# Kernel tuning notes

Measured on AMD Instinct MI355X. Metric: run time of the kernel, lower is better.

## Reference

```python
import jax, jax.numpy as jnp
import numpy as np

N_HEADS = 16
D_MODEL = 1024
D_K = 64
D_V = 64


def setup_inputs() -> dict:
    key = jax.random.key(0)
    ks = jax.random.split(key, 12)
    B, S = 2, 2048
    s = 0.02
    return {
        "q": jax.random.normal(ks[0], (B, S, D_MODEL), jnp.float32),
        "k": jax.random.normal(ks[1], (B, S, D_MODEL), jnp.float32),
        "v": jax.random.normal(ks[2], (B, S, D_MODEL), jnp.float32),
        "bias": jax.random.normal(ks[3], (B, N_HEADS, S, S), jnp.float32),
        "w_q": jax.random.normal(ks[4], (D_MODEL, N_HEADS * D_K), jnp.float32) * s,
        "b_q": jnp.zeros((N_HEADS * D_K,), jnp.float32),
        "w_k": jax.random.normal(ks[5], (D_MODEL, N_HEADS * D_K), jnp.float32) * s,
        "b_k": jnp.zeros((N_HEADS * D_K,), jnp.float32),
        "w_v": jax.random.normal(ks[6], (D_MODEL, N_HEADS * D_V), jnp.float32) * s,
        "b_v": jnp.zeros((N_HEADS * D_V,), jnp.float32),
        "w_o": jax.random.normal(ks[7], (D_MODEL, D_MODEL), jnp.float32) * s,
        "b_o": jnp.zeros((D_MODEL,), jnp.float32),
    }


def reference(q, k, v, bias, w_q, b_q, w_k, b_k, w_v, b_v, w_o, b_o):
    B, Sq, _ = q.shape
    Sk = k.shape[1]
    # QKV projections -> [B, H, S, d]
    qh = (q @ w_q + b_q).reshape(B, Sq, N_HEADS, D_K).transpose(0, 2, 1, 3)
    kh = (k @ w_k + b_k).reshape(B, Sk, N_HEADS, D_K).transpose(0, 2, 1, 3)
    vh = (v @ w_v + b_v).reshape(B, Sk, N_HEADS, D_V).transpose(0, 2, 1, 3)
    scale = 1.0 / jnp.sqrt(jnp.asarray(D_K, qh.dtype))
    attn = jnp.einsum("bhqd,bhkd->bhqk", qh * scale, kh) + bias
    weights = jax.nn.softmax(attn, axis=-1)  # dropout=0 -> identity
    out = jnp.einsum("bhqk,bhkd->bhqd", weights, vh)
    out = out.transpose(0, 2, 1, 3).reshape(B, Sq, N_HEADS * D_V)
    return out @ w_o + b_o
```

## Files before the change

### kernel.cpp

```cpp
#include <hip/hip_runtime.h>
#include <stdint.h>

#define H_ 16
#define B_ 2
#define S_ 2048
#define DMODEL 1024
#define MTOT 4096

typedef __attribute__((ext_vector_type(8))) __bf16 bf16x8;
typedef __attribute__((ext_vector_type(4))) float f32x4;
typedef unsigned short ushort_t;

typedef __attribute__((address_space(1))) uint32_t u32_g;
typedef __attribute__((address_space(3))) uint32_t u32_l;

static __device__ __forceinline__ unsigned short f2bf(float f) {
  union { float f; uint32_t u; } x; x.f = f;
  uint32_t r = (x.u + 0x7FFFu + ((x.u >> 16) & 1u)) >> 16;
  return (unsigned short)r;
}

static __device__ __forceinline__ void gld_lds16(const void* g, void* l) {
  __builtin_amdgcn_global_load_lds((const u32_g*)g, (u32_l*)l, 16, 0, 0);
}

__global__ __launch_bounds__(256) void cast_qkv(const float* __restrict__ q,
                                                const float* __restrict__ k,
                                                const float* __restrict__ v,
                                                ushort_t* qb, ushort_t* kb, ushort_t* vb) {
  int z = blockIdx.y;
  const float* src = (z == 0) ? q : (z == 1) ? k : v;
  ushort_t* dst = (z == 0) ? qb : (z == 1) ? kb : vb;
  int idx = (blockIdx.x * 256 + threadIdx.x) * 4;
  float4 f = *(const float4*)(src + idx);
  ushort4 o;
  o.x = f2bf(f.x); o.y = f2bf(f.y); o.z = f2bf(f.z); o.w = f2bf(f.w);
  *(ushort4*)(dst + idx) = o;
}

__global__ __launch_bounds__(256) void transw(const float* __restrict__ wq, const float* __restrict__ wk,
                                              const float* __restrict__ wv, const float* __restrict__ wo,
                                              ushort_t* tq, ushort_t* tk, ushort_t* tv, ushort_t* tow) {
  int z = blockIdx.y;
  const float* src = (z == 0) ? wq : (z == 1) ? wk : (z == 2) ? wv : wo;
  ushort_t* dst = (z == 0) ? tq : (z == 1) ? tk : (z == 2) ? tv : tow;
  __shared__ ushort_t lds[64 * 65];
  int t = threadIdx.x;
  int k0 = (blockIdx.x & 15) * 64;
  int n0 = (blockIdx.x >> 4) * 64;
  int r = t >> 4;
  int c4 = (t & 15) * 4;
#pragma unroll
  for (int j = 0; j < 4; ++j) {
    int row = j * 16 + r;
    float4 f = *(const float4*)(src + (size_t)(k0 + row) * DMODEL + n0 + c4);
    lds[(c4 + 0) * 65 + row] = f2bf(f.x);
    lds[(c4 + 1) * 65 + row] = f2bf(f.y);
    lds[(c4 + 2) * 65 + row] = f2bf(f.z);
    lds[(c4 + 3) * 65 + row] = f2bf(f.w);
  }
  __syncthreads();
  int nn = t >> 2;
  int kb = (t & 3) * 16;
  ushort_t tmp[16];
#pragma unroll
  for (int j = 0; j < 16; ++j) tmp[j] = lds[nn * 65 + kb + j];
  ushort_t* dp = dst + (size_t)(n0 + nn) * DMODEL + k0 + kb;
  *(uint4*)(dp + 0) = *(const uint4*)(tmp + 0);
  *(uint4*)(dp + 8) = *(const uint4*)(tmp + 8);
}

struct GemmArgs {
  const ushort_t* A;
  const ushort_t* Bt;
  const float* bias;
  void* out;
  int mode;
  float mult;
};

__global__ __launch_bounds__(256) void gemm128(GemmArgs g0, GemmArgs g1, GemmArgs g2) {
  GemmArgs ga = (blockIdx.z == 0) ? g0 : (blockIdx.z == 1) ? g1 : g2;
  __shared__ alignas(16) ushort_t smem[2][128 * 64];
  ushort_t* As = smem[0];
  ushort_t* Bs = smem[1];
  int tid = threadIdx.x, wid = tid >> 6, lane = tid & 63;
  int lg = lane >> 4, li = lane & 15;
  int wr = wid >> 1, wc = wid & 1;
  int m0 = blockIdx.y * 128, n0 = blockIdx.x * 128;
  f32x4 acc[4][4] = {};
  const ushort_t* Ab = ga.A + (size_t)m0 * DMODEL;
  const ushort_t* Bb = ga.Bt + (size_t)n0 * DMODEL;

  for (int kt = 0; kt < DMODEL / 64; ++kt) {
    int k0 = kt * 64;
    __syncthreads();
#pragma unroll
    for (int r = 0; r < 4; ++r) {
      int c = r * 256 + tid;
      int row = c >> 3, off = (c & 7) * 8;
      gld_lds16(Ab + row * DMODEL + k0 + off, (char*)As + c * 16);
      gld_lds16(Bb + row * DMODEL + k0 + off, (char*)Bs + c * 16);
    }
    __syncthreads();
#pragma unroll
    for (int kk = 0; kk < 2; ++kk) {
      bf16x8 af[4], bfr[4];
#pragma unroll
      for (int x = 0; x < 4; ++x) {
        af[x]  = *(const bf16x8*)(As + (wr * 64 + x * 16 + li) * 64 + kk * 32 + lg * 8);
        bfr[x] = *(const bf16x8*)(Bs + (wc * 64 + x * 16 + li) * 64 + kk * 32 + lg * 8);
      }
#pragma unroll
      for (int mi = 0; mi < 4; ++mi)
#pragma unroll
        for (int ni = 0; ni < 4; ++ni)
          acc[mi][ni] = __builtin_amdgcn_mfma_f32_16x16x32_bf16(af[mi], bfr[ni], acc[mi][ni], 0, 0, 0);
    }
  }

  if (ga.mode == 1) {
    __syncthreads();
    ushort_t* ep = &smem[0][0];
#pragma unroll
    for (int mi = 0; mi < 4; ++mi)
#pragma unroll
      for (int ni = 0; ni < 4; ++ni) {
        int nl = wc * 64 + ni * 16 + li;
        float bv = ga.bias[n0 + nl];
#pragma unroll
        for (int i = 0; i < 4; ++i) {
          int ml = wr * 64 + mi * 16 + lg * 4 + i;
          ep[nl * 128 + ml] = f2bf((acc[mi][ni][i] + bv) * ga.mult);
        }
      }
    __syncthreads();
    int row = tid >> 1;
    int cg  = (tid & 1) * 64;
    int n = n0 + row;
    int h = n >> 6, d = n & 63;
    int b = m0 >> 11;
    size_t base = ((size_t)(b * H_ + h) * 64 + d) * S_ + (m0 & 2047) + cg;
    ushort_t* out = (ushort_t*)ga.out;
    const ushort_t* sp = ep + row * 128 + cg;
#pragma unroll
    for (int j = 0; j < 8; ++j)
      *(uint4*)(out + base + j * 8) = *(const uint4*)(sp + j * 8);
  } else {
#pragma unroll
    for (int mi = 0; mi < 4; ++mi) {
#pragma unroll
      for (int ni = 0; ni < 4; ++ni) {
        int n = n0 + wc * 64 + ni * 16 + li;
        float bv = ga.bias[n];
#pragma unroll
        for (int i = 0; i < 4; ++i) {
          int m = m0 + wr * 64 + mi * 16 + lg * 4 + i;
          float val = (acc[mi][ni][i] + bv) * ga.mult;
          if (ga.mode == 2) {
            ((float*)ga.out)[(size_t)m * DMODEL + n] = val;
          } else {
            int b = m >> 11, s = m & 2047;
            int h = n >> 6, d = n & 63;
            size_t addr = ((size_t)(b * H_ + h) * S_ + s) * 64 + d;
            ((ushort_t*)ga.out)[addr] = f2bf(val);
          }
        }
      }
    }
  }
}

__global__ __launch_bounds__(256, 4) void attn(const ushort_t* __restrict__ Qh,
                                               const ushort_t* __restrict__ Kh,
                                               const ushort_t* __restrict__ VhT,
                                               const float* __restrict__ bias,
                                               ushort_t* __restrict__ attnO) {
  int qt = blockIdx.x * 64;
  int h = blockIdx.y, b = blockIdx.z;
  int tid = threadIdx.x, wid = tid >> 6, lane = tid & 63;
  int lg = lane >> 4, li = lane & 15;
  __shared__ alignas(16) ushort_t Ks[2][64 * 64];
  __shared__ alignas(16) ushort_t Vts[2][64 * 64];
  __shared__ alignas(16) ushort_t Ps[4][16][64];

  const size_t bh = (size_t)(b * H_ + h);
  const ushort_t* Qbase = Qh + bh * S_ * 64;
  const ushort_t* Kbase = Kh + bh * S_ * 64;
  const ushort_t* Vbase = VhT + bh * 64 * S_;
  const float* biasb = bias + bh * (size_t)S_ * S_;
  const int qrow = qt + wid * 16 + lg * 4;

  bf16x8 qf[2];
#pragma unroll
  for (int kk = 0; kk < 2; ++kk)
    qf[kk] = *(const bf16x8*)(Qbase + (size_t)(qt + wid * 16 + li) * 64 + kk * 32 + lg * 8);

  auto stage = [&](int buf, int t) {
#pragma unroll
    for (int r = 0; r < 2; ++r) {
      int cc = r * 256 + tid;
      int row = cc >> 3, off = (cc & 7) * 8;
      gld_lds16(Kbase + (size_t)(t * 64 + row) * 64 + off, (char*)Ks[buf] + cc * 16);
      gld_lds16(Vbase + (size_t)row * S_ + t * 64 + off, (char*)Vts[buf] + cc * 16);
    }
  };
  auto biasld = [&](float (&dst)[4][4], int t) {
#pragma unroll
    for (int n = 0; n < 4; ++n)
#pragma unroll
      for (int i = 0; i < 4; ++i)
        dst[n][i] = biasb[(size_t)(qrow + i) * S_ + t * 64 + n * 16 + li];
  };

  f32x4 o[4] = {};
  float mrow[4] = {-3.0e38f, -3.0e38f, -3.0e38f, -3.0e38f};
  float lrow[4] = {0.f, 0.f, 0.f, 0.f};
  float bsvN[4][4], bsvC[4][4];

  stage(0, 0);
  biasld(bsvN, 0);

  for (int t = 0; t < S_ / 64; ++t) {
    __syncthreads();
#pragma unroll
    for (int n = 0; n < 4; ++n)
#pragma unroll
      for (int i = 0; i < 4; ++i)
        bsvC[n][i] = bsvN[n][i];
    if (t + 1 < S_ / 64) {
      stage((t + 1) & 1, t + 1);
      biasld(bsvN, t + 1);
    }
    const ushort_t* Kc = Ks[t & 1];
    const ushort_t* Vc = Vts[t & 1];

    f32x4 sc[4] = {};
#pragma unroll
    for (int kk = 0; kk < 2; ++kk) {
#pragma unroll
      for (int n = 0; n < 4; ++n) {
        bf16x8 bk = *(const bf16x8*)(Kc + (n * 16 + li) * 64 + kk * 32 + lg * 8);
        sc[n] = __builtin_amdgcn_mfma_f32_16x16x32_bf16(qf[kk], bk, sc[n], 0, 0, 0);
      }
    }
#pragma unroll
    for (int n = 0; n < 4; ++n)
#pragma unroll
      for (int i = 0; i < 4; ++i)
        sc[n][i] += bsvC[n][i];

    float p[4][4];
#pragma unroll
    for (int i = 0; i < 4; ++i) {
      float tm = fmaxf(fmaxf(sc[0][i], sc[1][i]), fmaxf(sc[2][i], sc[3][i]));
#pragma unroll
      for (int w = 1; w < 16; w <<= 1) tm = fmaxf(tm, __shfl_xor(tm, w));
      float mn = fmaxf(mrow[i], tm);
      float alpha = __expf(mrow[i] - mn);
      float rs = 0.f;
#pragma unroll
      for (int n = 0; n < 4; ++n) { p[n][i] = __expf(sc[n][i] - mn); rs += p[n][i]; }
#pragma unroll
      for (int w = 1; w < 16; w <<= 1) rs += __shfl_xor(rs, w);
      lrow[i] = lrow[i] * alpha + rs;
      mrow[i] = mn;
#pragma unroll
      for (int n = 0; n < 4; ++n) o[n][i] *= alpha;
    }

#pragma unroll
    for (int n = 0; n < 4; ++n)
#pragma unroll
      for (int i = 0; i < 4; ++i)
        Ps[wid][lg * 4 + i][n * 16 + li] = f2bf(p[n][i]);

#pragma unroll
    for (int kk = 0; kk < 2; ++kk) {
      bf16x8 pa = *(const bf16x8*)(&Ps[wid][li][kk * 32 + lg * 8]);
#pragma unroll
      for (int n = 0; n < 4; ++n) {
        bf16x8 bv = *(const bf16x8*)(Vc + (n * 16 + li) * 64 + kk * 32 + lg * 8);
        o[n] = __builtin_amdgcn_mfma_f32_16x16x32_bf16(pa, bv, o[n], 0, 0, 0);
      }
    }
  }

  float rinv[4];
#pragma unroll
  for (int i = 0; i < 4; ++i) rinv[i] = 1.0f / lrow[i];
#pragma unroll
  for (int n = 0; n < 4; ++n)
#pragma unroll
    for (int i = 0; i < 4; ++i) {
      int q = qt + wid * 16 + lg * 4 + i;
      int col = h * 64 + n * 16 + li;
      attnO[(size_t)(b * S_ + q) * DMODEL + col] = f2bf(o[n][i] * rinv[i]);
    }
}

extern "C" void kernel_launch(void* const* d_in, const int* in_sizes, int n_in,
                              void* d_out, int out_size, void* d_ws, size_t ws_size,
                              hipStream_t stream) {
  const float* q    = (const float*)d_in[0];
  const float* k    = (const float*)d_in[1];
  const float* v    = (const float*)d_in[2];
  const float* bias = (const float*)d_in[3];
  const float* w_q  = (const float*)d_in[4];
  const float* b_q  = (const float*)d_in[5];
  const float* w_k  = (const float*)d_in[6];
  const float* b_k  = (const float*)d_in[7];
  const float* w_v  = (const float*)d_in[8];
  const float* b_v  = (const float*)d_in[9];
  const float* w_o  = (const float*)d_in[10];
  const float* b_o  = (const float*)d_in[11];

  char* ws = (char*)d_ws;
  const size_t MB = 1ull << 20;
  ushort_t* qb  = (ushort_t*)(ws + 0 * MB);
  ushort_t* kb  = (ushort_t*)(ws + 8 * MB);
  ushort_t* vb  = (ushort_t*)(ws + 16 * MB);
  ushort_t* wqT = (ushort_t*)(ws + 24 * MB);
  ushort_t* wkT = (ushort_t*)(ws + 26 * MB);
  ushort_t* wvT = (ushort_t*)(ws + 28 * MB);
  ushort_t* woT = (ushort_t*)(ws + 30 * MB);
  ushort_t* Qh  = (ushort_t*)(ws + 32 * MB);
  ushort_t* Kh  = (ushort_t*)(ws + 40 * MB);
  ushort_t* VhT = (ushort_t*)(ws + 48 * MB);
  ushort_t* aO  = qb;

  cast_qkv<<<dim3(4096, 3, 1), 256, 0, stream>>>(q, k, v, qb, kb, vb);
  transw<<<dim3(256, 4, 1), 256, 0, stream>>>(w_q, w_k, w_v, w_o, wqT, wkT, wvT, woT);

  GemmArgs gq { qb, wqT, b_q, (void*)Qh,  0, 0.125f };
  GemmArgs gk { kb, wkT, b_k, (void*)Kh,  0, 1.0f };
  GemmArgs gv { vb, wvT, b_v, (void*)VhT, 1, 1.0f };
  gemm128<<<dim3(8, 32, 3), 256, 0, stream>>>(gq, gk, gv);

  attn<<<dim3(32, 16, 2), 256, 0, stream>>>(Qh, Kh, VhT, bias, aO);

  GemmArgs go { aO, woT, b_o, d_out, 2, 1.0f };
  gemm128<<<dim3(8, 32, 1), 256, 0, stream>>>(go, go, go);
}
```

Before: 884.3 us.

## XOR-swizzle attention LDS tiles and add dedicated output-projection GEMM kernel

The attention kernel now XOR-swizzles the K, V and P shared-memory tiles by row, applied both on the global-to-LDS loads and on the MFMA fragment reads. This is meant to remove LDS bank conflicts on the 16-byte fragment reads. The output projection moves from the generic 128x128 GEMM to a new 64x128-tile kernel, which doubles the block count (512 blocks) for better occupancy. The new kernel has no double buffering, and the generic GEMM loses its fp32 output mode.

Result: no change. 881.9 us (-0.3%).

```diff
diff --git a/kernel.cpp b/kernel.cpp
--- a/kernel.cpp
+++ b/kernel.cpp
@@ -157,18 +157,73 @@
         for (int i = 0; i < 4; ++i) {
           int m = m0 + wr * 64 + mi * 16 + lg * 4 + i;
           float val = (acc[mi][ni][i] + bv) * ga.mult;
-          if (ga.mode == 2) {
-            ((float*)ga.out)[(size_t)m * DMODEL + n] = val;
-          } else {
-            int b = m >> 11, s = m & 2047;
-            int h = n >> 6, d = n & 63;
-            size_t addr = ((size_t)(b * H_ + h) * S_ + s) * 64 + d;
-            ((ushort_t*)ga.out)[addr] = f2bf(val);
-          }
+          int b = m >> 11, s = m & 2047;
+          int h = n >> 6, d = n & 63;
+          size_t addr = ((size_t)(b * H_ + h) * S_ + s) * 64 + d;
+          ((ushort_t*)ga.out)[addr] = f2bf(val);
         }
       }
     }
   }
+}
+
+__global__ __launch_bounds__(256) void gemm_out(const ushort_t* __restrict__ A,
+                                                const ushort_t* __restrict__ Bt,
+                                                const float* __restrict__ bias,
+                                                float* __restrict__ out) {
+  __shared__ alignas(16) ushort_t As[64 * 64];
+  __shared__ alignas(16) ushort_t Bs[128 * 64];
+  int tid = threadIdx.x, wid = tid >> 6, lane = tid & 63;
+  int lg = lane >> 4, li = lane & 15;
+  int m0 = blockIdx.y * 64, n0 = blockIdx.x * 128;
+  f32x4 acc[4][2] = {};
+  const ushort_t* Ab = A + (size_t)m0 * DMODEL;
+  const ushort_t* Bb = Bt + (size_t)n0 * DMODEL;
+
+  for (int kt = 0; kt < DMODEL / 64; ++kt) {
+    int k0 = kt * 64;
+    __syncthreads();
+#pragma unroll
+    for (int r = 0; r < 2; ++r) {
+      int c = r * 256 + tid;
+      int row = c >> 3, off = (c & 7) * 8;
+      gld_lds16(Ab + row * DMODEL + k0 + off, (char*)As + c * 16);
+    }
+#pragma unroll
+    for (int r = 0; r < 4; ++r) {
+      int c = r * 256 + tid;
+      int row = c >> 3, off = (c & 7) * 8;
+      gld_lds16(Bb + row * DMODEL + k0 + off, (char*)Bs + c * 16);
+    }
+    __syncthreads();
+#pragma unroll
+    for (int kk = 0; kk < 2; ++kk) {
+      bf16x8 af[4], bfr[2];
+#pragma unroll
+      for (int x = 0; x < 4; ++x)
+        af[x] = *(const bf16x8*)(As + (x * 16 + li) * 64 + kk * 32 + lg * 8);
+#pragma unroll
+      for (int x = 0; x < 2; ++x)
+        bfr[x] = *(const bf16x8*)(Bs + (wid * 32 + x * 16 + li) * 64 + kk * 32 + lg * 8);
+#pragma unroll
+      for (int mi = 0; mi < 4; ++mi)
+#pragma unroll
+        for (int ni = 0; ni < 2; ++ni)
+          acc[mi][ni] = __builtin_amdgcn_mfma_f32_16x16x32_bf16(af[mi], bfr[ni], acc[mi][ni], 0, 0, 0);
+    }
+  }
+#pragma unroll
+  for (int mi = 0; mi < 4; ++mi)
+#pragma unroll
+    for (int ni = 0; ni < 2; ++ni) {
+      int n = n0 + wid * 32 + ni * 16 + li;
+      float bv = bias[n];
+#pragma unroll
+      for (int i = 0; i < 4; ++i) {
+        int m = m0 + mi * 16 + lg * 4 + i;
+        out[(size_t)m * DMODEL + n] = acc[mi][ni][i] + bv;
+      }
+    }
 }
 
 __global__ __launch_bounds__(256, 4) void attn(const ushort_t* __restrict__ Qh,
@@ -182,7 +237,7 @@
   int lg = lane >> 4, li = lane & 15;
   __shared__ alignas(16) ushort_t Ks[2][64 * 64];
   __shared__ alignas(16) ushort_t Vts[2][64 * 64];
-  __shared__ alignas(16) ushort_t Ps[4][16][64];
+  __shared__ alignas(16) ushort_t Ps[4 * 16 * 64];
 
   const size_t bh = (size_t)(b * H_ + h);
   const ushort_t* Qbase = Qh + bh * S_ * 64;
@@ -200,7 +255,8 @@
 #pragma unroll
     for (int r = 0; r < 2; ++r) {
       int cc = r * 256 + tid;
-      int row = cc >> 3, off = (cc & 7) * 8;
+      int row = cc >> 3;
+      int off = ((cc & 7) ^ (row & 7)) * 8;
       gld_lds16(Kbase + (size_t)(t * 64 + row) * 64 + off, (char*)Ks[buf] + cc * 16);
       gld_lds16(Vbase + (size_t)row * S_ + t * 64 + off, (char*)Vts[buf] + cc * 16);
     }
@@ -240,7 +296,8 @@
     for (int kk = 0; kk < 2; ++kk) {
 #pragma unroll
       for (int n = 0; n < 4; ++n) {
-        bf16x8 bk = *(const bf16x8*)(Kc + (n * 16 + li) * 64 + kk * 32 + lg * 8);
+        int c8 = (kk * 4 + lg) ^ (li & 7);
+        bf16x8 bk = *(const bf16x8*)(Kc + (n * 16 + li) * 64 + c8 * 8);
         sc[n] = __builtin_amdgcn_mfma_f32_16x16x32_bf16(qf[kk], bk, sc[n], 0, 0, 0);
       }
     }
@@ -272,15 +329,20 @@
 #pragma unroll
     for (int n = 0; n < 4; ++n)
 #pragma unroll
-      for (int i = 0; i < 4; ++i)
-        Ps[wid][lg * 4 + i][n * 16 + li] = f2bf(p[n][i]);
+      for (int i = 0; i < 4; ++i) {
+        int r = lg * 4 + i;
+        int c8s = (n * 2 + (li >> 3)) ^ (r & 7);
+        Ps[wid * 1024 + r * 64 + c8s * 8 + (li & 7)] = f2bf(p[n][i]);
+      }
 
 #pragma unroll
     for (int kk = 0; kk < 2; ++kk) {
-      bf16x8 pa = *(const bf16x8*)(&Ps[wid][li][kk * 32 + lg * 8]);
+      int c8p = (kk * 4 + lg) ^ (li & 7);
+      bf16x8 pa = *(const bf16x8*)(Ps + wid * 1024 + li * 64 + c8p * 8);
 #pragma unroll
       for (int n = 0; n < 4; ++n) {
-        bf16x8 bv = *(const bf16x8*)(Vc + (n * 16 + li) * 64 + kk * 32 + lg * 8);
+        int c8 = (kk * 4 + lg) ^ (li & 7);
+        bf16x8 bv = *(const bf16x8*)(Vc + (n * 16 + li) * 64 + c8 * 8);
         o[n] = __builtin_amdgcn_mfma_f32_16x16x32_bf16(pa, bv, o[n], 0, 0, 0);
       }
     }
@@ -339,6 +401,5 @@
 
   attn<<<dim3(32, 16, 2), 256, 0, stream>>>(Qh, Kh, VhT, bias, aO);
 
-  GemmArgs go { aO, woT, b_o, d_out, 2, 1.0f };
-  gemm128<<<dim3(8, 32, 1), 256, 0, stream>>>(go, go, go);
-}
+  gemm_out<<<dim3(8, 64, 1), 256, 0, stream>>>(aO, woT, b_o, (float*)d_out);
+}
```
